# Performance work log

Hardware: AMD Instinct MI355X
Metric: run time of the kernel (lower is better)

Reference implementation:

```python
import jax, jax.numpy as jnp
import numpy as np
import math

D_MODEL = 1024
N_HEADS = 8
D_FF = 4 * D_MODEL
EPS = 1e-5


def layer_norm(x, g, b):
    mu = jnp.mean(x, axis=-1, keepdims=True)
    var = jnp.mean(jnp.square(x - mu), axis=-1, keepdims=True)
    return (x - mu) / jnp.sqrt(var + EPS) * g + b


def setup_inputs() -> dict:
    key = jax.random.key(0)
    ks = jax.random.split(key, 8)
    B, S = 1, 4096
    x = jax.random.normal(ks[0], (B, S, D_MODEL), dtype=jnp.float32)
    # linear params (stored as [in, out]); init scale ~ 1/sqrt(fan_in)
    qkv_w = jax.random.normal(ks[1], (D_MODEL, 3 * D_MODEL), dtype=jnp.float32) * (1.0 / math.sqrt(D_MODEL))
    qkv_b = jnp.zeros((3 * D_MODEL,), dtype=jnp.float32)
    w1 = jax.random.normal(ks[2], (D_MODEL, D_FF), dtype=jnp.float32) * (1.0 / math.sqrt(D_MODEL))
    b1 = jnp.zeros((D_FF,), dtype=jnp.float32)
    w2 = jax.random.normal(ks[3], (D_FF, D_MODEL), dtype=jnp.float32) * (1.0 / math.sqrt(D_FF))
    b2 = jnp.zeros((D_MODEL,), dtype=jnp.float32)
    ln1_g = jnp.ones((D_MODEL,), dtype=jnp.float32)
    ln1_b = jnp.zeros((D_MODEL,), dtype=jnp.float32)
    ln2_g = jnp.ones((D_MODEL,), dtype=jnp.float32)
    ln2_b = jnp.zeros((D_MODEL,), dtype=jnp.float32)
    return {"x": x, "ln1_g": ln1_g, "ln1_b": ln1_b, "qkv_w": qkv_w, "qkv_b": qkv_b,
            "ln2_g": ln2_g, "ln2_b": ln2_b, "w1": w1, "b1": b1, "w2": w2, "b2": b2}


def reference(x, ln1_g, ln1_b, qkv_w, qkv_b, ln2_g, ln2_b, w1, b1, w2, b2):
    B, S, D = x.shape
    hd = D // N_HEADS
    scaler = math.sqrt(hd)

    h = layer_norm(x, ln1_g, ln1_b)                       # [B,S,D]
    qkv = h @ qkv_w + qkv_b                               # [B,S,3D]
    q, k, v = jnp.split(qkv, 3, axis=-1)
    # b s (h d) -> b h s d
    def split_heads(t):
        return t.reshape(B, S, N_HEADS, hd).transpose(0, 2, 1, 3)
    q, k, v = split_heads(q), split_heads(k), split_heads(v)
    scores = jnp.einsum('bhqd,bhkd->bhqk', q, k) / scaler  # [B,H,S,S] materialized, as in source
    attn = jax.nn.softmax(scores, axis=-1)
    heads = jnp.einsum('bhqk,bhkd->bhqd', attn, v)        # [B,H,S,hd]
    attn_score = heads.transpose(0, 2, 1, 3).reshape(B, S, D)  # b h t d -> b t (h d)
    # NOTE: source returns attn_score (the proj Linear output is discarded)
    h = attn_score + h                                     # residual with ln1 output
    h = layer_norm(h, ln2_g, ln2_b)
    h = jax.nn.gelu(h @ w1 + b1, approximate=False) @ w2 + b2  # no final residual
    return h
```

## Files before the change

kernel.cpp:

```cpp
#include <hip/hip_runtime.h>
#include <stdint.h>


typedef __bf16 bf16;
typedef __attribute__((ext_vector_type(8))) __bf16 bf16x8;
typedef __attribute__((ext_vector_type(4))) __bf16 bf16x4;
typedef __attribute__((ext_vector_type(4))) float f32x4;

#define DEV static __device__ __forceinline__

#define QSCALE 0.12751741687f

DEV void gload_lds16(const void* gsrc, void* ldst) {
  typedef const __attribute__((address_space(1))) uint32_t gq_t;
  typedef __attribute__((address_space(3))) uint32_t lq_t;
  __builtin_amdgcn_global_load_lds((gq_t*)(uintptr_t)gsrc, (lq_t*)(uintptr_t)ldst,
                                   16, 0, 0);
}

DEV f32x4 mfma16(bf16x8 a, bf16x8 b, f32x4 c) {
  return __builtin_amdgcn_mfma_f32_16x16x32_bf16(a, b, c, 0, 0, 0);
}

__global__ __launch_bounds__(256) void pre_kernel(
    const float* __restrict__ x, const float* __restrict__ gw,
    const float* __restrict__ bw, bf16* __restrict__ hout,
    const float* __restrict__ qkv_w, bf16* __restrict__ wTq) {
  __shared__ float tile[32][33];
  __shared__ float red[8];
  int bid = blockIdx.x, t = threadIdx.x;
  if (bid < 4096) {
    int row = bid;
    const float* xr = x + (size_t)row * 1024;
    f32x4 v = *(const f32x4*)(xr + t * 4);
    float s = v[0] + v[1] + v[2] + v[3];
    float s2 = v[0] * v[0] + v[1] * v[1] + v[2] * v[2] + v[3] * v[3];
#pragma unroll
    for (int off = 1; off < 64; off <<= 1) {
      s += __shfl_xor(s, off);
      s2 += __shfl_xor(s2, off);
    }
    if ((t & 63) == 0) { red[t >> 6] = s; red[4 + (t >> 6)] = s2; }
    __syncthreads();
    s = red[0] + red[1] + red[2] + red[3];
    s2 = red[4] + red[5] + red[6] + red[7];
    float mu = s * (1.f / 1024.f);
    float rstd = rsqrtf(s2 * (1.f / 1024.f) - mu * mu + 1e-5f);
    f32x4 gv = *(const f32x4*)(gw + t * 4);
    f32x4 bv = *(const f32x4*)(bw + t * 4);
    bf16x4 o;
#pragma unroll
    for (int j = 0; j < 4; j++) o[j] = (bf16)((v[j] - mu) * rstd * gv[j] + bv[j]);
    *(bf16x4*)(hout + (size_t)row * 1024 + t * 4) = o;
  } else {
    int idx = bid - 4096;
    int c0 = (idx % 96) * 32, r0 = (idx / 96) * 32;
    int tx = t & 31, ty = t >> 5;
#pragma unroll
    for (int j = 0; j < 4; j++)
      tile[ty + 8 * j][tx] = qkv_w[(size_t)(r0 + ty + 8 * j) * 3072 + c0 + tx];
    __syncthreads();
#pragma unroll
    for (int j = 0; j < 4; j++)
      wTq[(size_t)(c0 + ty + 8 * j) * 1024 + r0 + tx] = (bf16)tile[tx][ty + 8 * j];
  }
}

__global__ __launch_bounds__(256) void mid_kernel(
    const float* __restrict__ w1, bf16* __restrict__ w1T,
    const float* __restrict__ w2, bf16* __restrict__ w2T,
    const bf16* __restrict__ Op, const float* __restrict__ lbuf,
    const bf16* __restrict__ h, const float* __restrict__ gw,
    const float* __restrict__ bw, bf16* __restrict__ out) {
  __shared__ float tile[32][33];
  __shared__ float red[8];
  int bid = blockIdx.x, t = threadIdx.x;
  if (bid < 8192) {
    const float* in; bf16* outp; int R, C, c0, r0;
    if (bid < 4096) {
      in = w1; outp = w1T; R = 1024; C = 4096;
      c0 = (bid & 127) * 32; r0 = (bid >> 7) * 32;
    } else {
      int idx = bid - 4096;
      in = w2; outp = w2T; R = 4096; C = 1024;
      c0 = (idx & 31) * 32; r0 = (idx >> 5) * 32;
    }
    int tx = t & 31, ty = t >> 5;
#pragma unroll
    for (int j = 0; j < 4; j++)
      tile[ty + 8 * j][tx] = in[(size_t)(r0 + ty + 8 * j) * C + c0 + tx];
    __syncthreads();
#pragma unroll
    for (int j = 0; j < 4; j++)
      outp[(size_t)(c0 + ty + 8 * j) * R + r0 + tx] = (bf16)tile[tx][ty + 8 * j];
  } else {
    int row = bid - 8192;
    int head = t >> 5;
    float l = 0.f;
    float acc[4] = {0.f, 0.f, 0.f, 0.f};
#pragma unroll
    for (int z = 0; z < 2; z++) {
      l += lbuf[(size_t)(z * 8 + head) * 4096 + row];
      bf16x4 ov = *(const bf16x4*)(Op + (size_t)z * 4096 * 1024 +
                                   (size_t)row * 1024 + t * 4);
#pragma unroll
      for (int j = 0; j < 4; j++) acc[j] += (float)ov[j];
    }
    float rl = 1.0f / l;
    bf16x4 hv = *(const bf16x4*)(h + (size_t)row * 1024 + t * 4);
    float vv[4];
#pragma unroll
    for (int j = 0; j < 4; j++) vv[j] = acc[j] * rl + (float)hv[j];
    float s = vv[0] + vv[1] + vv[2] + vv[3];
    float s2 = vv[0] * vv[0] + vv[1] * vv[1] + vv[2] * vv[2] + vv[3] * vv[3];
#pragma unroll
    for (int off = 1; off < 64; off <<= 1) {
      s += __shfl_xor(s, off);
      s2 += __shfl_xor(s2, off);
    }
    if ((t & 63) == 0) { red[t >> 6] = s; red[4 + (t >> 6)] = s2; }
    __syncthreads();
    s = red[0] + red[1] + red[2] + red[3];
    s2 = red[4] + red[5] + red[6] + red[7];
    float mu = s * (1.f / 1024.f);
    float rstd = rsqrtf(s2 * (1.f / 1024.f) - mu * mu + 1e-5f);
    f32x4 gv = *(const f32x4*)(gw + t * 4);
    f32x4 bv = *(const f32x4*)(bw + t * 4);
    bf16x4 o;
#pragma unroll
    for (int j = 0; j < 4; j++) o[j] = (bf16)((vv[j] - mu) * rstd * gv[j] + bv[j]);
    *(bf16x4*)(out + (size_t)row * 1024 + t * 4) = o;
  }
}

__global__ __launch_bounds__(256) void ffn2_combine_kernel(
    const bf16* __restrict__ P, const float* __restrict__ b2,
    float* __restrict__ out) {
  int row = blockIdx.x, t = threadIdx.x;
  float acc[4];
  f32x4 bv = *(const f32x4*)(b2 + t * 4);
#pragma unroll
  for (int j = 0; j < 4; j++) acc[j] = bv[j];
#pragma unroll
  for (int z = 0; z < 4; z++) {
    bf16x4 pv = *(const bf16x4*)(P + (size_t)z * 4096 * 1024 +
                                 (size_t)row * 1024 + t * 4);
#pragma unroll
    for (int j = 0; j < 4; j++) acc[j] += (float)pv[j];
  }
  f32x4 o = {acc[0], acc[1], acc[2], acc[3]};
  *(f32x4*)(out + (size_t)row * 1024 + t * 4) = o;
}

template <int EPILOG>
__global__ __launch_bounds__(512) void gemm8p_kernel(
    const bf16* __restrict__ A, const bf16* __restrict__ Bt,
    const float* __restrict__ bias, bf16* __restrict__ Cout,
    bf16* __restrict__ Vout, int M, int N, int K, int Ks) {
  extern __shared__ char smem[];
  if constexpr (EPILOG == 4) {
    size_t zo = (size_t)blockIdx.z * Ks;
    A += zo; Bt += zo;
    Cout += (size_t)blockIdx.z * ((size_t)M * N);
  }
  int nwg = gridDim.x * gridDim.y;
  int bid = blockIdx.y * gridDim.x + blockIdx.x;
  int swz = (bid & 7) * (nwg >> 3) + (bid >> 3);
  int bx = swz % gridDim.x, by = swz / gridDim.x;
  int m0 = by * 256, n0 = bx * 256;
  int tid = threadIdx.x, wave = tid >> 6, lane = tid & 63;
  int lr = lane & 15, lg = lane >> 4;
  int wr = (wave >> 2) * 128;
  int wc = (wave & 3) * 64;
  const int NT = Ks >> 6;

  f32x4 acc[8][4] = {};

  const int sArow = tid >> 3;
  const int scbA = ((tid & 7) * 16) ^ (((tid >> 3) & 7) << 4);
  const int scbB = ((lane & 7) * 16) ^ ((lane >> 3) << 4);

  auto stageA = [&](int c, int T) {
    char* sAb = smem + (size_t)(T & 1) * 32768;
#pragma unroll
    for (int j = 0; j < 2; j++) {
      int r0 = j * 128 + 64 * c;
      gload_lds16(A + (size_t)(m0 + r0 + sArow) * K + T * 64 + scbA / 2,
                  sAb + r0 * 128 + wave * 1024);
    }
  };
  auto stageB = [&](int c, int T) {
    char* sBb = smem + 65536 + (size_t)(T & 1) * 32768;
    int wrun = (wave >> 2) * 64 + 32 * c + (wave & 3) * 8;
#pragma unroll
    for (int j = 0; j < 2; j++) {
      int r0 = j * 128 + wrun;
      gload_lds16(Bt + (size_t)(n0 + r0 + (lane >> 3)) * K + T * 64 + scbB / 2,
                  sBb + r0 * 128);
    }
  };
  auto ldA = [&](bf16x8 (&af)[4][2], int qm, int b) {
    const char* sAb = smem + (size_t)b * 32768;
#pragma unroll
    for (int mm = 0; mm < 4; mm++)
#pragma unroll
      for (int kk = 0; kk < 2; kk++) {
        int rl = wr + 64 * qm + mm * 16 + lr;
        int db = (kk * 64 + lg * 16) ^ ((rl & 7) << 4);
        af[mm][kk] = *(const bf16x8*)(sAb + rl * 128 + db);
      }
  };
  auto ldB = [&](bf16x8 (&bfv)[2][2], int qn, int b) {
    const char* sBb = smem + 65536 + (size_t)b * 32768;
#pragma unroll
    for (int nn = 0; nn < 2; nn++)
#pragma unroll
      for (int kk = 0; kk < 2; kk++) {
        int rb = wc + 32 * qn + nn * 16 + lr;
        int db = (kk * 64 + lg * 16) ^ ((rb & 7) << 4);
        bfv[nn][kk] = *(const bf16x8*)(sBb + rb * 128 + db);
      }
  };
  auto mfmaQ = [&](bf16x8 (&af)[4][2], bf16x8 (&bfv)[2][2], int qm, int qn) {
    __builtin_amdgcn_s_setprio(1);
#pragma unroll
    for (int kk = 0; kk < 2; kk++)
#pragma unroll
      for (int mm = 0; mm < 4; mm++)
#pragma unroll
        for (int nn = 0; nn < 2; nn++)
          acc[qm * 4 + mm][qn * 2 + nn] =
              mfma16(af[mm][kk], bfv[nn][kk], acc[qm * 4 + mm][qn * 2 + nn]);
    __builtin_amdgcn_s_setprio(0);
  };

  stageA(0, 0); stageB(0, 0); stageA(1, 0); stageB(1, 0);
  stageA(0, 1); stageB(0, 1);
  asm volatile("s_waitcnt vmcnt(4)" ::: "memory");
  __builtin_amdgcn_s_barrier();

  for (int T = 0; T < NT; T++) {
    int b = T & 1;
    bf16x8 af[4][2], bfv[2][2];
    ldA(af, 0, b); ldB(bfv, 0, b);
    if (T + 1 < NT) stageA(1, T + 1);
    __builtin_amdgcn_s_barrier();
    mfmaQ(af, bfv, 0, 0);
    __builtin_amdgcn_s_barrier();
    ldB(bfv, 1, b);
    if (T + 1 < NT) stageB(1, T + 1);
    __builtin_amdgcn_s_barrier();
    mfmaQ(af, bfv, 0, 1);
    __builtin_amdgcn_s_barrier();
    ldA(af, 1, b); ldB(bfv, 0, b);
    if (T + 2 < NT) stageA(0, T + 2);
    __builtin_amdgcn_s_barrier();
    mfmaQ(af, bfv, 1, 0);
    __builtin_amdgcn_s_barrier();
    ldB(bfv, 1, b);
    if (T + 2 < NT) stageB(0, T + 2);
    __builtin_amdgcn_s_barrier();
    mfmaQ(af, bfv, 1, 1);
    if (T < NT - 2) asm volatile("s_waitcnt vmcnt(4)" ::: "memory");
    else            asm volatile("s_waitcnt vmcnt(0)" ::: "memory");
    __builtin_amdgcn_s_barrier();
  }

#pragma unroll
  for (int n = 0; n < 4; n++) {
    int col = n0 + wc + n * 16 + lr;
    float bs = (EPILOG == 4) ? 0.f : bias[col];
#pragma unroll
    for (int m = 0; m < 8; m++) {
      int row0 = m0 + wr + m * 16 + lg * 4;
      if constexpr (EPILOG == 3) {
        if (col >= 2048) {
          bf16x4 pk;
#pragma unroll
          for (int r = 0; r < 4; r++) pk[r] = (bf16)(acc[m][n][r] + bs);
          *(bf16x4*)(Vout + (size_t)(col - 2048) * 4096 + row0) = pk;
          continue;
        }
      }
#pragma unroll
      for (int r = 0; r < 4; r++) {
        float v = acc[m][n][r] + bs;
        if constexpr (EPILOG == 1) {
          float u = v + 0.044715f * v * v * v;
          float e = __builtin_amdgcn_exp2f(-2.3021144f * u);
          v = v / (1.0f + e);
        }
        if constexpr (EPILOG == 3) { if (col < 1024) v *= QSCALE; }
        Cout[(size_t)(row0 + r) * N + col] = (bf16)v;
      }
    }
  }
}

__global__ __launch_bounds__(256) void attn_kernel(
    const bf16* __restrict__ qkv, const bf16* __restrict__ vt,
    bf16* __restrict__ opart, float* __restrict__ lbuf) {
  constexpr int S = 4096, C3 = 3072;
  extern __shared__ char asmem[];
  int hh = blockIdx.y;
  int q0 = blockIdx.x * 128;
  int z = blockIdx.z;
  int kv_begin = z * (S / 2), kv_end = kv_begin + (S / 2);
  bf16* obuf = opart + (size_t)z * 4096 * 1024;
  int tid = threadIdx.x, wave = tid >> 6, lane = tid & 63;
  int lr = lane & 15, lg = lane >> 4;

  bf16x8 qf[2][4];
#pragma unroll
  for (int qs = 0; qs < 2; qs++) {
    const bf16* qrow =
        qkv + (size_t)(q0 + wave * 32 + qs * 16 + lr) * C3 + hh * 128 + lg * 8;
#pragma unroll
    for (int kk = 0; kk < 4; kk++) qf[qs][kk] = *(const bf16x8*)(qrow + kk * 32);
  }
  f32x4 o[2][8] = {};
  float lsum[2] = {0.f, 0.f};

  const int krow_s = tid >> 4;
  const int kcb = (tid & 15) * 16;
  const int scbK = kcb ^ ((krow_s & 7) << 4);
  const int vrow_s = tid >> 3;
  const int vcb = (tid & 7) * 16;
  const int scbV = vcb ^ ((vrow_s & 7) << 4);

  const bf16* kbase = qkv + 1024 + hh * 128 + scbK / 2;
  const bf16* vbase = vt + (size_t)(hh * 128 + vrow_s) * S + scbV / 2;

  char* pw = asmem + 65536 + wave * 4096;

#define STAGE(B, KV0)                                                        \
  do {                                                                       \
    _Pragma("unroll") for (int i = 0; i < 4; i++)                            \
        gload_lds16(kbase + (size_t)((KV0) + i * 16 + krow_s) * C3,          \
                    asmem + (B) * 16384 + i * 4096 + wave * 1024);           \
    _Pragma("unroll") for (int i = 0; i < 4; i++)                            \
        gload_lds16(vbase + (size_t)(i * 32) * S + (KV0),                    \
                    asmem + 32768 + (B) * 16384 + i * 4096 + wave * 1024);   \
  } while (0)

  STAGE(0, kv_begin);
  __syncthreads();
  int buf = 0;

  for (int kv0 = kv_begin; kv0 < kv_end; kv0 += 64) {
    if (kv0 + 64 < kv_end) STAGE(buf ^ 1, kv0 + 64);

    const char* sKb = asmem + buf * 16384;
    const char* sVb = asmem + 32768 + buf * 16384;

#pragma unroll
    for (int nfp = 0; nfp < 2; nfp++) {
      f32x4 s00 = {0.f, 0.f, 0.f, 0.f}, s01 = s00, s10 = s00, s11 = s00;
      __builtin_amdgcn_s_setprio(1);
#pragma unroll
      for (int kk = 0; kk < 4; kk++) {
        int kr0 = (nfp * 2 + 0) * 16 + lr;
        int kr1 = (nfp * 2 + 1) * 16 + lr;
        int db0 = (kk * 64 + lg * 16) ^ ((kr0 & 7) << 4);
        int db1 = (kk * 64 + lg * 16) ^ ((kr1 & 7) << 4);
        bf16x8 kf0 = *(const bf16x8*)(sKb + kr0 * 256 + db0);
        bf16x8 kf1 = *(const bf16x8*)(sKb + kr1 * 256 + db1);
        s00 = mfma16(kf0, qf[0][kk], s00);
        s01 = mfma16(kf0, qf[1][kk], s01);
        s10 = mfma16(kf1, qf[0][kk], s10);
        s11 = mfma16(kf1, qf[1][kk], s11);
      }
      __builtin_amdgcn_s_setprio(0);
      f32x4 scs[2][2] = {{s00, s01}, {s10, s11}};
#pragma unroll
      for (int nfh = 0; nfh < 2; nfh++) {
        int nf = nfp * 2 + nfh;
#pragma unroll
        for (int qs = 0; qs < 2; qs++) {
          float p0 = __builtin_amdgcn_exp2f(scs[nfh][qs][0]);
          float p1 = __builtin_amdgcn_exp2f(scs[nfh][qs][1]);
          float p2 = __builtin_amdgcn_exp2f(scs[nfh][qs][2]);
          float p3 = __builtin_amdgcn_exp2f(scs[nfh][qs][3]);
          lsum[qs] += (p0 + p1) + (p2 + p3);
          bf16x4 pk;
          pk[0] = (bf16)p0; pk[1] = (bf16)p1; pk[2] = (bf16)p2; pk[3] = (bf16)p3;
          *(bf16x4*)(pw + (qs * 16 + lr) * 128 +
                     ((nf * 32 + lg * 8) ^ ((lr & 7) << 4))) = pk;
        }
      }
    }

    bf16x8 pa[2][2];
#pragma unroll
    for (int qs = 0; qs < 2; qs++)
#pragma unroll
      for (int kk = 0; kk < 2; kk++) {
        int db = (kk * 64 + lg * 16) ^ ((lr & 7) << 4);
        pa[qs][kk] = *(const bf16x8*)(pw + (qs * 16 + lr) * 128 + db);
      }
    __builtin_amdgcn_s_setprio(1);
#pragma unroll
    for (int df = 0; df < 8; df++) {
#pragma unroll
      for (int kk = 0; kk < 2; kk++) {
        int vrow = df * 16 + lr;
        int db = (kk * 64 + lg * 16) ^ ((vrow & 7) << 4);
        bf16x8 vf = *(const bf16x8*)(sVb + vrow * 128 + db);
        o[0][df] = mfma16(pa[0][kk], vf, o[0][df]);
        o[1][df] = mfma16(pa[1][kk], vf, o[1][df]);
      }
    }
    __builtin_amdgcn_s_setprio(0);
    __syncthreads();
    buf ^= 1;
  }
#undef STAGE

#pragma unroll
  for (int qs = 0; qs < 2; qs++) {
    float ls = lsum[qs];
    ls += __shfl_xor(ls, 16);
    ls += __shfl_xor(ls, 32);
    if (lg == 0)
      lbuf[(size_t)(z * 8 + hh) * 4096 + q0 + wave * 32 + qs * 16 + lr] = ls;
#pragma unroll
    for (int df = 0; df < 8; df++) {
      int col = hh * 128 + df * 16 + lr;
#pragma unroll
      for (int r = 0; r < 4; r++) {
        int row = q0 + wave * 32 + qs * 16 + lg * 4 + r;
        obuf[(size_t)row * 1024 + col] = (bf16)o[qs][df][r];
      }
    }
  }
}

extern "C" void kernel_launch(void* const* d_in, const int* in_sizes, int n_in,
                              void* d_out, int out_size, void* d_ws, size_t ws_size,
                              hipStream_t stream) {
  const float* x     = (const float*)d_in[0];
  const float* ln1_g = (const float*)d_in[1];
  const float* ln1_b = (const float*)d_in[2];
  const float* qkv_w = (const float*)d_in[3];
  const float* qkv_b = (const float*)d_in[4];
  const float* ln2_g = (const float*)d_in[5];
  const float* ln2_b = (const float*)d_in[6];
  const float* w1    = (const float*)d_in[7];
  const float* b1    = (const float*)d_in[8];
  const float* w2    = (const float*)d_in[9];
  const float* b2    = (const float*)d_in[10];

  char* ws = (char*)d_ws;
  const size_t MB = 1ull << 20;
  bf16*  h     = (bf16*)(ws + 0);
  bf16*  qkv   = (bf16*)(ws + 8 * MB);
  bf16*  h2    = (bf16*)(ws + 8 * MB);
  bf16*  w1T   = (bf16*)(ws + 16 * MB);
  bf16*  fpart = (bf16*)(ws + 0);
  bf16*  vt    = (bf16*)(ws + 32 * MB);
  bf16*  w2T   = (bf16*)(ws + 32 * MB);
  bf16*  Op    = (bf16*)(ws + 40 * MB);
  bf16*  ffn1  = (bf16*)(ws + 40 * MB);
  float* lbuf  = (float*)(ws + 72 * MB);
  bf16*  wTq   = (bf16*)(ws + 72 * MB + 512 * 1024);
  float* outp  = (float*)d_out;

  hipFuncSetAttribute(reinterpret_cast<const void*>(gemm8p_kernel<3>),
                      hipFuncAttributeMaxDynamicSharedMemorySize, 131072);
  hipFuncSetAttribute(reinterpret_cast<const void*>(gemm8p_kernel<1>),
                      hipFuncAttributeMaxDynamicSharedMemorySize, 131072);
  hipFuncSetAttribute(reinterpret_cast<const void*>(gemm8p_kernel<4>),
                      hipFuncAttributeMaxDynamicSharedMemorySize, 131072);
  hipFuncSetAttribute(reinterpret_cast<const void*>(attn_kernel),
                      hipFuncAttributeMaxDynamicSharedMemorySize, 81920);

  pre_kernel<<<7168, 256, 0, stream>>>(x, ln1_g, ln1_b, h, qkv_w, wTq);
  gemm8p_kernel<3><<<dim3(3072 / 256, 4096 / 256), 512, 131072, stream>>>(
      h, wTq, qkv_b, qkv, vt, 4096, 3072, 1024, 1024);
  attn_kernel<<<dim3(32, 8, 2), 256, 81920, stream>>>(qkv, vt, Op, lbuf);
  mid_kernel<<<12288, 256, 0, stream>>>(w1, w1T, w2, w2T, Op, lbuf, h,
                                        ln2_g, ln2_b, h2);
  gemm8p_kernel<1><<<dim3(4096 / 256, 4096 / 256), 512, 131072, stream>>>(
      h2, w1T, b1, ffn1, nullptr, 4096, 4096, 1024, 1024);
  gemm8p_kernel<4><<<dim3(1024 / 256, 4096 / 256, 4), 512, 131072, stream>>>(
      ffn1, w2T, nullptr, fpart, nullptr, 4096, 1024, 4096, 1024);
  ffn2_combine_kernel<<<4096, 256, 0, stream>>>(fpart, b2, outp);
}
```

Measured before the change: 232.6 us.

## Overlap W1/W2 transpose with QKV GEMM using spare workgroups

The W1/W2 fp32-to-bf16 transposes move out of the mid kernel and into 64 extra workgroups appended to the QKV GEMM launch (192 GEMM tiles plus 64 transpose blocks on 256 CUs). The aim is to fill idle compute units during the QKV GEMM so the transpose is hidden, leaving mid_kernel as a pure LN2 pass. The workspace layout is reshuffled so the transposed weights do not overlap live buffers. The split-K FFN2 is now issued as two launches (one slice, then three), so the first partial can go to a free region. Transpose blocks loop over 64 tiles each, which may lengthen the tail of the GEMM launch.

```diff
diff --git a/kernel.cpp b/kernel.cpp
--- a/kernel.cpp
+++ b/kernel.cpp
@@ -67,83 +67,64 @@
 }
 
 __global__ __launch_bounds__(256) void mid_kernel(
-    const float* __restrict__ w1, bf16* __restrict__ w1T,
-    const float* __restrict__ w2, bf16* __restrict__ w2T,
     const bf16* __restrict__ Op, const float* __restrict__ lbuf,
     const bf16* __restrict__ h, const float* __restrict__ gw,
     const float* __restrict__ bw, bf16* __restrict__ out) {
-  __shared__ float tile[32][33];
   __shared__ float red[8];
-  int bid = blockIdx.x, t = threadIdx.x;
-  if (bid < 8192) {
-    const float* in; bf16* outp; int R, C, c0, r0;
-    if (bid < 4096) {
-      in = w1; outp = w1T; R = 1024; C = 4096;
-      c0 = (bid & 127) * 32; r0 = (bid >> 7) * 32;
-    } else {
-      int idx = bid - 4096;
-      in = w2; outp = w2T; R = 4096; C = 1024;
-      c0 = (idx & 31) * 32; r0 = (idx >> 5) * 32;
-    }
-    int tx = t & 31, ty = t >> 5;
-#pragma unroll
-    for (int j = 0; j < 4; j++)
-      tile[ty + 8 * j][tx] = in[(size_t)(r0 + ty + 8 * j) * C + c0 + tx];
-    __syncthreads();
-#pragma unroll
-    for (int j = 0; j < 4; j++)
-      outp[(size_t)(c0 + ty + 8 * j) * R + r0 + tx] = (bf16)tile[tx][ty + 8 * j];
-  } else {
-    int row = bid - 8192;
-    int head = t >> 5;
-    float l = 0.f;
-    float acc[4] = {0.f, 0.f, 0.f, 0.f};
-#pragma unroll
-    for (int z = 0; z < 2; z++) {
-      l += lbuf[(size_t)(z * 8 + head) * 4096 + row];
-      bf16x4 ov = *(const bf16x4*)(Op + (size_t)z * 4096 * 1024 +
-                                   (size_t)row * 1024 + t * 4);
-#pragma unroll
-      for (int j = 0; j < 4; j++) acc[j] += (float)ov[j];
-    }
-    float rl = 1.0f / l;
-    bf16x4 hv = *(const bf16x4*)(h + (size_t)row * 1024 + t * 4);
-    float vv[4];
-#pragma unroll
-    for (int j = 0; j < 4; j++) vv[j] = acc[j] * rl + (float)hv[j];
-    float s = vv[0] + vv[1] + vv[2] + vv[3];
-    float s2 = vv[0] * vv[0] + vv[1] * vv[1] + vv[2] * vv[2] + vv[3] * vv[3];
-#pragma unroll
-    for (int off = 1; off < 64; off <<= 1) {
-      s += __shfl_xor(s, off);
-      s2 += __shfl_xor(s2, off);
-    }
-    if ((t & 63) == 0) { red[t >> 6] = s; red[4 + (t >> 6)] = s2; }
-    __syncthreads();
-    s = red[0] + red[1] + red[2] + red[3];
-    s2 = red[4] + red[5] + red[6] + red[7];
-    float mu = s * (1.f / 1024.f);
-    float rstd = rsqrtf(s2 * (1.f / 1024.f) - mu * mu + 1e-5f);
-    f32x4 gv = *(const f32x4*)(gw + t * 4);
-    f32x4 bv = *(const f32x4*)(bw + t * 4);
-    bf16x4 o;
-#pragma unroll
-    for (int j = 0; j < 4; j++) o[j] = (bf16)((vv[j] - mu) * rstd * gv[j] + bv[j]);
-    *(bf16x4*)(out + (size_t)row * 1024 + t * 4) = o;
-  }
+  int row = blockIdx.x, t = threadIdx.x;
+  int head = t >> 5;
+  float l = 0.f;
+  float acc[4] = {0.f, 0.f, 0.f, 0.f};
+#pragma unroll
+  for (int z = 0; z < 2; z++) {
+    l += lbuf[(size_t)(z * 8 + head) * 4096 + row];
+    bf16x4 ov = *(const bf16x4*)(Op + (size_t)z * 4096 * 1024 +
+                                 (size_t)row * 1024 + t * 4);
+#pragma unroll
+    for (int j = 0; j < 4; j++) acc[j] += (float)ov[j];
+  }
+  float rl = 1.0f / l;
+  bf16x4 hv = *(const bf16x4*)(h + (size_t)row * 1024 + t * 4);
+  float vv[4];
+#pragma unroll
+  for (int j = 0; j < 4; j++) vv[j] = acc[j] * rl + (float)hv[j];
+  float s = vv[0] + vv[1] + vv[2] + vv[3];
+  float s2 = vv[0] * vv[0] + vv[1] * vv[1] + vv[2] * vv[2] + vv[3] * vv[3];
+#pragma unroll
+  for (int off = 1; off < 64; off <<= 1) {
+    s += __shfl_xor(s, off);
+    s2 += __shfl_xor(s2, off);
+  }
+  if ((t & 63) == 0) { red[t >> 6] = s; red[4 + (t >> 6)] = s2; }
+  __syncthreads();
+  s = red[0] + red[1] + red[2] + red[3];
+  s2 = red[4] + red[5] + red[6] + red[7];
+  float mu = s * (1.f / 1024.f);
+  float rstd = rsqrtf(s2 * (1.f / 1024.f) - mu * mu + 1e-5f);
+  f32x4 gv = *(const f32x4*)(gw + t * 4);
+  f32x4 bv = *(const f32x4*)(bw + t * 4);
+  bf16x4 o;
+#pragma unroll
+  for (int j = 0; j < 4; j++) o[j] = (bf16)((vv[j] - mu) * rstd * gv[j] + bv[j]);
+  *(bf16x4*)(out + (size_t)row * 1024 + t * 4) = o;
 }
 
 __global__ __launch_bounds__(256) void ffn2_combine_kernel(
-    const bf16* __restrict__ P, const float* __restrict__ b2,
-    float* __restrict__ out) {
+    const bf16* __restrict__ P0, const bf16* __restrict__ P123,
+    const float* __restrict__ b2, float* __restrict__ out) {
   int row = blockIdx.x, t = threadIdx.x;
   float acc[4];
   f32x4 bv = *(const f32x4*)(b2 + t * 4);
 #pragma unroll
   for (int j = 0; j < 4; j++) acc[j] = bv[j];
-#pragma unroll
-  for (int z = 0; z < 4; z++) {
-    bf16x4 pv = *(const bf16x4*)(P + (size_t)z * 4096 * 1024 +
+  {
+    bf16x4 pv = *(const bf16x4*)(P0 + (size_t)row * 1024 + t * 4);
+#pragma unroll
+    for (int j = 0; j < 4; j++) acc[j] += (float)pv[j];
+  }
+#pragma unroll
+  for (int z = 0; z < 3; z++) {
+    bf16x4 pv = *(const bf16x4*)(P123 + (size_t)z * 4096 * 1024 +
                                  (size_t)row * 1024 + t * 4);
 #pragma unroll
     for (int j = 0; j < 4; j++) acc[j] += (float)pv[j];
@@ -156,17 +137,54 @@
 __global__ __launch_bounds__(512) void gemm8p_kernel(
     const bf16* __restrict__ A, const bf16* __restrict__ Bt,
     const float* __restrict__ bias, bf16* __restrict__ Cout,
-    bf16* __restrict__ Vout, int M, int N, int K, int Ks) {
+    bf16* __restrict__ Vout, int M, int N, int K, int Ks,
+    const float* __restrict__ w1, bf16* __restrict__ w1T,
+    const float* __restrict__ w2, bf16* __restrict__ w2T) {
   extern __shared__ char smem[];
-  if constexpr (EPILOG == 4) {
-    size_t zo = (size_t)blockIdx.z * Ks;
-    A += zo; Bt += zo;
-    Cout += (size_t)blockIdx.z * ((size_t)M * N);
-  }
-  int nwg = gridDim.x * gridDim.y;
-  int bid = blockIdx.y * gridDim.x + blockIdx.x;
-  int swz = (bid & 7) * (nwg >> 3) + (bid >> 3);
-  int bx = swz % gridDim.x, by = swz / gridDim.x;
+  int bx, by;
+  if constexpr (EPILOG == 3) {
+    int bid = blockIdx.x;
+    if (bid >= 192) {
+      int t = threadIdx.x & 255, half = threadIdx.x >> 8;
+      float* tl = (float*)(smem + half * 4352);
+      int tx = t & 31, ty = t >> 5;
+      for (int it = 0; it < 64; it++) {
+        int tile_idx = (bid - 192) * 128 + it * 2 + half;
+        const float* in; bf16* out; int R, C, c0, r0;
+        if (tile_idx < 4096) {
+          in = w1; out = w1T; R = 1024; C = 4096;
+          c0 = (tile_idx & 127) * 32; r0 = (tile_idx >> 7) * 32;
+        } else {
+          int i2 = tile_idx - 4096;
+          in = w2; out = w2T; R = 4096; C = 1024;
+          c0 = (i2 & 31) * 32; r0 = (i2 >> 5) * 32;
+        }
+#pragma unroll
+        for (int j = 0; j < 4; j++)
+          tl[(ty + 8 * j) * 33 + tx] =
+              in[(size_t)(r0 + ty + 8 * j) * C + c0 + tx];
+        __syncthreads();
+#pragma unroll
+        for (int j = 0; j < 4; j++)
+          out[(size_t)(c0 + ty + 8 * j) * R + r0 + tx] =
+              (bf16)tl[tx * 33 + ty + 8 * j];
+        __syncthreads();
+      }
+      return;
+    }
+    int swz = (bid & 7) * 24 + (bid >> 3);
+    bx = swz % 12; by = swz / 12;
+  } else {
+    if constexpr (EPILOG == 4) {
+      size_t zo = (size_t)blockIdx.z * Ks;
+      A += zo; Bt += zo;
+      Cout += (size_t)blockIdx.z * ((size_t)M * N);
+    }
+    int nwg = gridDim.x * gridDim.y;
+    int bid = blockIdx.y * gridDim.x + blockIdx.x;
+    int swz = (bid & 7) * (nwg >> 3) + (bid >> 3);
+    bx = swz % gridDim.x; by = swz / gridDim.x;
+  }
   int m0 = by * 256, n0 = bx * 256;
   int tid = threadIdx.x, wave = tid >> 6, lane = tid & 63;
   int lr = lane & 15, lg = lane >> 4;
@@ -453,14 +471,15 @@
   char* ws = (char*)d_ws;
   const size_t MB = 1ull << 20;
   bf16*  h     = (bf16*)(ws + 0);
+  bf16*  h2    = (bf16*)(ws + 0);
+  bf16*  fp0   = (bf16*)(ws + 0);
   bf16*  qkv   = (bf16*)(ws + 8 * MB);
-  bf16*  h2    = (bf16*)(ws + 8 * MB);
-  bf16*  w1T   = (bf16*)(ws + 16 * MB);
-  bf16*  fpart = (bf16*)(ws + 0);
+  bf16*  ffn1  = (bf16*)(ws + 8 * MB);
   bf16*  vt    = (bf16*)(ws + 32 * MB);
-  bf16*  w2T   = (bf16*)(ws + 32 * MB);
   bf16*  Op    = (bf16*)(ws + 40 * MB);
-  bf16*  ffn1  = (bf16*)(ws + 40 * MB);
+  bf16*  fp123 = (bf16*)(ws + 40 * MB);
+  bf16*  w1T   = (bf16*)(ws + 56 * MB);
+  bf16*  w2T   = (bf16*)(ws + 64 * MB);
   float* lbuf  = (float*)(ws + 72 * MB);
   bf16*  wTq   = (bf16*)(ws + 72 * MB + 512 * 1024);
   float* outp  = (float*)d_out;
@@ -475,14 +494,18 @@
                       hipFuncAttributeMaxDynamicSharedMemorySize, 81920);
 
   pre_kernel<<<7168, 256, 0, stream>>>(x, ln1_g, ln1_b, h, qkv_w, wTq);
-  gemm8p_kernel<3><<<dim3(3072 / 256, 4096 / 256), 512, 131072, stream>>>(
-      h, wTq, qkv_b, qkv, vt, 4096, 3072, 1024, 1024);
+  gemm8p_kernel<3><<<256, 512, 131072, stream>>>(
+      h, wTq, qkv_b, qkv, vt, 4096, 3072, 1024, 1024, w1, w1T, w2, w2T);
   attn_kernel<<<dim3(32, 8, 2), 256, 81920, stream>>>(qkv, vt, Op, lbuf);
-  mid_kernel<<<12288, 256, 0, stream>>>(w1, w1T, w2, w2T, Op, lbuf, h,
-                                        ln2_g, ln2_b, h2);
+  mid_kernel<<<4096, 256, 0, stream>>>(Op, lbuf, h, ln2_g, ln2_b, h2);
   gemm8p_kernel<1><<<dim3(4096 / 256, 4096 / 256), 512, 131072, stream>>>(
-      h2, w1T, b1, ffn1, nullptr, 4096, 4096, 1024, 1024);
-  gemm8p_kernel<4><<<dim3(1024 / 256, 4096 / 256, 4), 512, 131072, stream>>>(
-      ffn1, w2T, nullptr, fpart, nullptr, 4096, 1024, 4096, 1024);
-  ffn2_combine_kernel<<<4096, 256, 0, stream>>>(fpart, b2, outp);
-}
+      h2, w1T, b1, ffn1, nullptr, 4096, 4096, 1024, 1024,
+      nullptr, nullptr, nullptr, nullptr);
+  gemm8p_kernel<4><<<dim3(1024 / 256, 4096 / 256, 1), 512, 131072, stream>>>(
+      ffn1, w2T, nullptr, fp0, nullptr, 4096, 1024, 4096, 1024,
+      nullptr, nullptr, nullptr, nullptr);
+  gemm8p_kernel<4><<<dim3(1024 / 256, 4096 / 256, 3), 512, 131072, stream>>>(
+      ffn1 + 1024, w2T + 1024, nullptr, fp123, nullptr, 4096, 1024, 4096, 1024,
+      nullptr, nullptr, nullptr, nullptr);
+  ffn2_combine_kernel<<<4096, 256, 0, stream>>>(fp0, fp123, b2, outp);
+}
```

After: 258.7 us. +11.2%, slower.
